# Kernel tuning notes

Hardware: AMD Instinct MI355X
Metric: run time of the kernel (lower is better)

Reference implementation:

```python
import jax, jax.numpy as jnp
import numpy as np

H, W, DIM, B, K = 28, 28, 384, 64, 1
EPS = 1e-5


def setup_inputs() -> dict:
    key = jax.random.key(0)
    k1, k2, k3 = jax.random.split(key, 3)
    L = 1 + K * H * W
    x = jax.random.normal(k1, (B, L, DIM), dtype=jnp.float32)
    w_reduction = jax.random.normal(k2, (2 * DIM, 4 * DIM), dtype=jnp.float32) * 0.02
    w_convert = jax.random.normal(k3, (2 * DIM, DIM), dtype=jnp.float32) * 0.02
    ln_gamma = jnp.ones((4 * DIM,), dtype=jnp.float32)
    ln_beta = jnp.zeros((4 * DIM,), dtype=jnp.float32)
    return {"x": x, "w_reduction": w_reduction, "w_convert": w_convert,
            "ln_gamma": ln_gamma, "ln_beta": ln_beta}


def reference(x, w_reduction, w_convert, ln_gamma, ln_beta):
    Bb, L, C = x.shape
    k = (L - 1) // (H * W)
    cls_token = x[:, 0:1, :]                      # [B,1,C]
    feat = x[:, 1:, :].reshape(Bb, k, H, W, C)
    x0 = feat[:, :, 0::2, 0::2, :]                # [B,k,H/2,W/2,C]
    x1 = feat[:, :, 1::2, 0::2, :]
    x2 = feat[:, :, 0::2, 1::2, :]
    x3 = feat[:, :, 1::2, 1::2, :]
    m = jnp.concatenate([x0, x1, x2, x3], axis=-1)  # [B,k,H/2,W/2,4C]
    m = m.reshape(Bb, k, -1, 4 * C)
    # LayerNorm over last dim
    mu = jnp.mean(m, axis=-1, keepdims=True)
    var = jnp.mean(jnp.square(m - mu), axis=-1, keepdims=True)
    m = (m - mu) * jax.lax.rsqrt(var + EPS) * ln_gamma + ln_beta
    red = jnp.einsum('bknf,of->bkno', m, w_reduction).reshape(Bb, -1, 2 * C)
    cls_out = jnp.einsum('bic,oc->bio', cls_token, w_convert)  # [B,1,2C]
    return jnp.concatenate([cls_out, red], axis=1)
```

## Files before the change

### kernel.cpp

```cpp
#include <hip/hip_runtime.h>
#include <hip/hip_bf16.h>

#define DIMC 384
#define LL 785
#define FDIM 1536
#define ODIM 768
#define NPATCH 196
#define MROWS 12544
#define BATCH 64

typedef __attribute__((ext_vector_type(8))) short bf16x8;
typedef __attribute__((ext_vector_type(4))) float floatx4;
typedef __attribute__((ext_vector_type(4))) unsigned short ushort4v;

#define WS_WBF_OFF  38535168
#define WS_PST_OFF  40894464
#define WS_B2_OFF   41295872

#define PB_CLS   0
#define PB_CAST  192
#define PB_BIAS  3328
#define PB_WBF   3520
#define PREP_BLOCKS 4672

__device__ __forceinline__ unsigned short f2bf(float f) {
  union { float f; unsigned int u; } v; v.f = f;
  unsigned int u = v.u + 0x7fffu + ((v.u >> 16) & 1u);
  return (unsigned short)(u >> 16);
}

__device__ __forceinline__ void gload_lds16(const void* g, void* l) {
  __builtin_amdgcn_global_load_lds(
      (const __attribute__((address_space(1))) unsigned int*)g,
      (__attribute__((address_space(3))) unsigned int*)l, 16, 0, 0);
}

__global__ __launch_bounds__(256) void prep_kernel(
    const float* __restrict__ x, const float* __restrict__ wred,
    const float* __restrict__ wconv, const float* __restrict__ gamma,
    const float* __restrict__ beta, unsigned short* __restrict__ xbf,
    unsigned short* __restrict__ wbf, float2* __restrict__ pst,
    float2* __restrict__ bias2, float* __restrict__ out) {
  const int blk = blockIdx.x;
  const int t = threadIdx.x;
  const int wv = t >> 6;
  const int lane = t & 63;

  if (blk >= PB_CAST && blk < PB_BIAS) {
    const int w = (blk - PB_CAST) * 4 + wv;
    const int vid = w * 4 + (lane >> 4);
    const int sub = lane & 15;
    const int b = vid / 784;
    const int ll = vid - b * 784;
    const float* src = x + ((size_t)b * LL + 1 + ll) * DIMC;
    unsigned short* dst = xbf + (size_t)vid * DIMC;
    float s = 0.f, s2 = 0.f;
#pragma unroll
    for (int c = 0; c < 6; ++c) {
      int f = sub * 4 + c * 64;
      float4 v = *reinterpret_cast<const float4*>(src + f);
      s  += v.x + v.y + v.z + v.w;
      s2 += v.x * v.x + v.y * v.y + v.z * v.z + v.w * v.w;
      union { ushort4v u4; __hip_bfloat162 h[2]; } u;
      u.h[0] = __float22bfloat162_rn(make_float2(v.x, v.y));
      u.h[1] = __float22bfloat162_rn(make_float2(v.z, v.w));
      *reinterpret_cast<ushort4v*>(dst + f) = u.u4;
    }
#pragma unroll
    for (int o = 1; o < 16; o <<= 1) {
      s  += __shfl_xor(s, o);
      s2 += __shfl_xor(s2, o);
    }
    if (sub == 0) pst[vid] = make_float2(s, s2);
  } else if (blk < PB_CAST) {
    __shared__ float xs[DIMC];
    int idx = blk;
    int b = idx / 3;
    int ch = idx - b * 3;
    for (int c = t; c < DIMC; c += 256) xs[c] = x[(size_t)b * LL * DIMC + c];
    __syncthreads();
    int o = ch * 256 + t;
    const float* wr = wconv + (size_t)o * DIMC;
    float a0 = 0.f, a1 = 0.f;
#pragma unroll 4
    for (int c = 0; c < DIMC; c += 8) {
      float4 w0 = *reinterpret_cast<const float4*>(wr + c);
      float4 w1 = *reinterpret_cast<const float4*>(wr + c + 4);
      float4 p0 = *reinterpret_cast<const float4*>(&xs[c]);
      float4 p1 = *reinterpret_cast<const float4*>(&xs[c + 4]);
      a0 += w0.x * p0.x + w0.y * p0.y + w0.z * p0.z + w0.w * p0.w;
      a1 += w1.x * p1.x + w1.y * p1.y + w1.z * p1.z + w1.w * p1.w;
    }
    out[(size_t)b * 197 * ODIM + o] = a0 + a1;
  } else if (blk < PB_WBF) {
    int o = (blk - PB_BIAS) * 4 + wv;
    const float* wr = wred + (size_t)o * FDIM;
    float sb = 0.f, sg = 0.f;
#pragma unroll
    for (int c = 0; c < 6; ++c) {
      int f = lane * 4 + c * 256;
      float4 w = *reinterpret_cast<const float4*>(wr + f);
      float4 be = *reinterpret_cast<const float4*>(beta + f);
      float4 ga = *reinterpret_cast<const float4*>(gamma + f);
      sb += w.x * be.x + w.y * be.y + w.z * be.z + w.w * be.w;
      sg += w.x * ga.x + w.y * ga.y + w.z * ga.z + w.w * ga.w;
    }
#pragma unroll
    for (int o2 = 32; o2 > 0; o2 >>= 1) {
      sb += __shfl_down(sb, o2);
      sg += __shfl_down(sg, o2);
    }
    if (lane == 0) bias2[o] = make_float2(sg, sb);
  } else {
    int idx4 = (blk - PB_WBF) * 256 + t;
    int e0 = idx4 * 4;
    int f = e0 % FDIM;
    float4 w = *reinterpret_cast<const float4*>(wred + e0);
    float4 g = *reinterpret_cast<const float4*>(gamma + f);
    ushort4v u;
    u.x = f2bf(w.x * g.x); u.y = f2bf(w.y * g.y);
    u.z = f2bf(w.z * g.z); u.w = f2bf(w.w * g.w);
    *reinterpret_cast<ushort4v*>(wbf + e0) = u;
  }
}

__global__ __launch_bounds__(256) void gemm_kernel(
    const unsigned short* __restrict__ xbf,
    const unsigned short* __restrict__ wbf,
    const float2* __restrict__ pst, const float2* __restrict__ bias2,
    float* __restrict__ out) {
  __shared__ unsigned short As[128 * 64];
  __shared__ unsigned short Bs[128 * 64];
  __shared__ float2 st[128];

  const int t = threadIdx.x;

  const int NWG = (ODIM / 128) * (MROWS / 128);
  const int qq = NWG >> 3, rr = NWG & 7;
  int bid = blockIdx.x;
  int xcd = bid & 7, pos = bid >> 3;
  int wg = (xcd < rr) ? xcd * (qq + 1) + pos
                      : rr * (qq + 1) + (xcd - rr) * qq + pos;
  int my = wg / 6;
  int nx = wg - my * 6;
  const int mBase = my * 128;
  const int nBase = nx * 128;

  if (t < 128) {
    int m = mBase + t;
    int b = m / NPATCH;
    int n = m - b * NPATCH;
    int i = n / 14;
    int j = n - i * 14;
    int base = b * 784 + i * 56 + j * 2;
    float2 p0 = pst[base];
    float2 p1 = pst[base + 28];
    float2 p2 = pst[base + 1];
    float2 p3 = pst[base + 29];
    float s = p0.x + p1.x + p2.x + p3.x;
    float s2 = p0.y + p1.y + p2.y + p3.y;
    float mu = s * (1.f / FDIM);
    float var = s2 * (1.f / FDIM) - mu * mu;
    float rs = rsqrtf(var + 1e-5f);
    st[t] = make_float2(rs, -mu * rs);
  }

  const unsigned short* agp[4];
  const unsigned short* bgp[4];
  unsigned int ldsoff[4];
#pragma unroll
  for (int p = 0; p < 4; ++p) {
    int s = p * 256 + t;
    int r = s >> 3;
    int cs = (s & 7) ^ (r & 7);
    int m = mBase + r;
    int b = m / NPATCH;
    int n = m - b * NPATCH;
    int i = n / 14;
    int j = n - i * 14;
    agp[p] = xbf + ((size_t)b * 784 + i * 56 + j * 2) * DIMC + cs * 8;
    bgp[p] = wbf + (size_t)(nBase + r) * FDIM + cs * 8;
    ldsoff[p] = (unsigned)s * 8;
  }

  const int wv = t >> 6;
  const int lane = t & 63;
  const int ln15 = lane & 15;
  const int quad = lane >> 4;
  const int wm = wv >> 1;
  const int wn = wv & 1;

  unsigned int aoff[4][2], boff[4][2];
#pragma unroll
  for (int mt = 0; mt < 4; ++mt) {
#pragma unroll
    for (int h = 0; h < 2; ++h) {
      int rA = wm * 64 + mt * 16 + ln15;
      aoff[mt][h] = (unsigned)(rA * 64 + (((h * 4 + quad) ^ (rA & 7)) * 8));
      int rB = wn * 64 + mt * 16 + ln15;
      boff[mt][h] = (unsigned)(rB * 64 + (((h * 4 + quad) ^ (rB & 7)) * 8));
    }
  }

  floatx4 acc[4][4];
#pragma unroll
  for (int mt = 0; mt < 4; ++mt)
#pragma unroll
    for (int nt = 0; nt < 4; ++nt)
      acc[mt][nt] = floatx4{0.f, 0.f, 0.f, 0.f};

  for (int kt = 0; kt < FDIM / 64; ++kt) {
    int q = kt / 6;
    int kk = kt - q * 6;
    int ao = ((q & 1) * 28 + ((q >> 1) & 1)) * DIMC + kk * 64;
    if (kt) __syncthreads();
#pragma unroll
    for (int p = 0; p < 4; ++p) {
      gload_lds16(agp[p] + ao, &As[ldsoff[p]]);
      gload_lds16(bgp[p], &Bs[ldsoff[p]]);
      bgp[p] += 64;
    }
    __syncthreads();

#pragma unroll
    for (int h = 0; h < 2; ++h) {
      bf16x8 af[4], bfr[4];
#pragma unroll
      for (int mt = 0; mt < 4; ++mt)
        af[mt] = *reinterpret_cast<const bf16x8*>(&As[aoff[mt][h]]);
#pragma unroll
      for (int nt = 0; nt < 4; ++nt)
        bfr[nt] = *reinterpret_cast<const bf16x8*>(&Bs[boff[nt][h]]);
#pragma unroll
      for (int mt = 0; mt < 4; ++mt)
#pragma unroll
        for (int nt = 0; nt < 4; ++nt)
          acc[mt][nt] = __builtin_amdgcn_mfma_f32_16x16x32_bf16(
              af[mt], bfr[nt], acc[mt][nt], 0, 0, 0);
    }
  }

  float2 gb[4];
#pragma unroll
  for (int nt = 0; nt < 4; ++nt)
    gb[nt] = bias2[nBase + wn * 64 + nt * 16 + ln15];
#pragma unroll
  for (int mt = 0; mt < 4; ++mt) {
#pragma unroll
    for (int r = 0; r < 4; ++r) {
      int rloc = wm * 64 + mt * 16 + quad * 4 + r;
      float2 sn = st[rloc];
      int m = mBase + rloc;
      int b = m / NPATCH;
      int n = m - b * NPATCH;
      float* orow = out + ((size_t)b * 197 + 1 + n) * ODIM + nBase + wn * 64;
#pragma unroll
      for (int nt = 0; nt < 4; ++nt) {
        float val = fmaf(acc[mt][nt][r], sn.x,
                         fmaf(sn.y, gb[nt].x, gb[nt].y));
        __builtin_nontemporal_store(val, &orow[nt * 16 + ln15]);
      }
    }
  }
}

extern "C" void kernel_launch(void* const* d_in, const int* in_sizes, int n_in,
                              void* d_out, int out_size, void* d_ws, size_t ws_size,
                              hipStream_t stream) {
  const float* x     = (const float*)d_in[0];
  const float* wred  = (const float*)d_in[1];
  const float* wconv = (const float*)d_in[2];
  const float* gamma = (const float*)d_in[3];
  const float* beta  = (const float*)d_in[4];
  float* out = (float*)d_out;

  unsigned short* xbf = (unsigned short*)d_ws;
  unsigned short* wbf = (unsigned short*)((char*)d_ws + WS_WBF_OFF);
  float2* pst         = (float2*)((char*)d_ws + WS_PST_OFF);
  float2* bias2       = (float2*)((char*)d_ws + WS_B2_OFF);

  prep_kernel<<<dim3(PREP_BLOCKS), 256, 0, stream>>>(x, wred, wconv, gamma,
                                                     beta, xbf, wbf, pst,
                                                     bias2, out);
  gemm_kernel<<<dim3((ODIM / 128) * (MROWS / 128)), 256, 0, stream>>>(
      xbf, wbf, pst, bias2, out);
}
```

Before: 174.1 us.

## Shrink GEMM N-tile to 64 for more workgroups; cast two rows per lane-group

The GEMM output tile goes from 128x128 to 128x64, doubling the workgroup count from 588 to 1176 so the 256 CUs are better filled, with a simplified XCD-aware mapping. Per-wave accumulators drop from 16 to 8 MFMA tiles, and the B LDS buffer is halved. Separately, the prep cast kernel now handles two rows per 16-lane group: it issues all loads before the bf16 stores and writes the paired stats as one float4, halving the block count. The smaller tile means more A-tile reloads, so the A matrix is fetched twice as often overall, and there is less MFMA work per LDS load.

```diff
diff --git a/kernel.cpp b/kernel.cpp
--- a/kernel.cpp
+++ b/kernel.cpp
@@ -19,9 +19,9 @@
 
 #define PB_CLS   0
 #define PB_CAST  192
-#define PB_BIAS  3328
-#define PB_WBF   3520
-#define PREP_BLOCKS 4672
+#define PB_BIAS  1760
+#define PB_WBF   1952
+#define PREP_BLOCKS 3104
 
 __device__ __forceinline__ unsigned short f2bf(float f) {
   union { float f; unsigned int u; } v; v.f = f;
@@ -48,30 +48,49 @@
 
   if (blk >= PB_CAST && blk < PB_BIAS) {
     const int w = (blk - PB_CAST) * 4 + wv;
-    const int vid = w * 4 + (lane >> 4);
+    const int vid0 = w * 8 + (lane >> 4) * 2;
     const int sub = lane & 15;
-    const int b = vid / 784;
-    const int ll = vid - b * 784;
-    const float* src = x + ((size_t)b * LL + 1 + ll) * DIMC;
-    unsigned short* dst = xbf + (size_t)vid * DIMC;
-    float s = 0.f, s2 = 0.f;
-#pragma unroll
-    for (int c = 0; c < 6; ++c) {
-      int f = sub * 4 + c * 64;
-      float4 v = *reinterpret_cast<const float4*>(src + f);
-      s  += v.x + v.y + v.z + v.w;
-      s2 += v.x * v.x + v.y * v.y + v.z * v.z + v.w * v.w;
-      union { ushort4v u4; __hip_bfloat162 h[2]; } u;
-      u.h[0] = __float22bfloat162_rn(make_float2(v.x, v.y));
-      u.h[1] = __float22bfloat162_rn(make_float2(v.z, v.w));
-      *reinterpret_cast<ushort4v*>(dst + f) = u.u4;
+    float4 v[2][6];
+    float s[2], s2[2];
+#pragma unroll
+    for (int r = 0; r < 2; ++r) {
+      int vid = vid0 + r;
+      int b = vid / 784;
+      int ll = vid - b * 784;
+      const float* src = x + ((size_t)b * LL + 1 + ll) * DIMC;
+      s[r] = 0.f; s2[r] = 0.f;
+#pragma unroll
+      for (int c = 0; c < 6; ++c) {
+        float4 vv = *reinterpret_cast<const float4*>(src + sub * 4 + c * 64);
+        v[r][c] = vv;
+        s[r]  += vv.x + vv.y + vv.z + vv.w;
+        s2[r] += vv.x * vv.x + vv.y * vv.y + vv.z * vv.z + vv.w * vv.w;
+      }
+    }
+#pragma unroll
+    for (int r = 0; r < 2; ++r) {
+      unsigned short* dst = xbf + (size_t)(vid0 + r) * DIMC;
+#pragma unroll
+      for (int c = 0; c < 6; ++c) {
+        float4 vv = v[r][c];
+        union { ushort4v u4; __hip_bfloat162 h[2]; } u;
+        u.h[0] = __float22bfloat162_rn(make_float2(vv.x, vv.y));
+        u.h[1] = __float22bfloat162_rn(make_float2(vv.z, vv.w));
+        *reinterpret_cast<ushort4v*>(dst + sub * 4 + c * 64) = u.u4;
+      }
     }
 #pragma unroll
     for (int o = 1; o < 16; o <<= 1) {
-      s  += __shfl_xor(s, o);
-      s2 += __shfl_xor(s2, o);
-    }
-    if (sub == 0) pst[vid] = make_float2(s, s2);
+#pragma unroll
+      for (int r = 0; r < 2; ++r) {
+        s[r]  += __shfl_xor(s[r], o);
+        s2[r] += __shfl_xor(s2[r], o);
+      }
+    }
+    if (sub == 0) {
+      float4 pp = make_float4(s[0], s2[0], s[1], s2[1]);
+      *reinterpret_cast<float4*>(&pst[vid0]) = pp;
+    }
   } else if (blk < PB_CAST) {
     __shared__ float xs[DIMC];
     int idx = blk;
@@ -130,21 +149,17 @@
     const float2* __restrict__ pst, const float2* __restrict__ bias2,
     float* __restrict__ out) {
   __shared__ unsigned short As[128 * 64];
-  __shared__ unsigned short Bs[128 * 64];
+  __shared__ unsigned short Bs[64 * 64];
   __shared__ float2 st[128];
 
   const int t = threadIdx.x;
 
-  const int NWG = (ODIM / 128) * (MROWS / 128);
-  const int qq = NWG >> 3, rr = NWG & 7;
   int bid = blockIdx.x;
-  int xcd = bid & 7, pos = bid >> 3;
-  int wg = (xcd < rr) ? xcd * (qq + 1) + pos
-                      : rr * (qq + 1) + (xcd - rr) * qq + pos;
-  int my = wg / 6;
-  int nx = wg - my * 6;
+  int wg = (bid & 7) * 147 + (bid >> 3);
+  int my = wg / 12;
+  int nx = wg - my * 12;
   const int mBase = my * 128;
-  const int nBase = nx * 128;
+  const int nBase = nx * 64;
 
   if (t < 128) {
     int m = mBase + t;
@@ -166,8 +181,8 @@
   }
 
   const unsigned short* agp[4];
-  const unsigned short* bgp[4];
-  unsigned int ldsoff[4];
+  const unsigned short* bgp[2];
+  unsigned int aldso[4], bldso[2];
 #pragma unroll
   for (int p = 0; p < 4; ++p) {
     int s = p * 256 + t;
@@ -179,8 +194,15 @@
     int i = n / 14;
     int j = n - i * 14;
     agp[p] = xbf + ((size_t)b * 784 + i * 56 + j * 2) * DIMC + cs * 8;
+    aldso[p] = (unsigned)s * 8;
+  }
+#pragma unroll
+  for (int p = 0; p < 2; ++p) {
+    int s = p * 256 + t;
+    int r = s >> 3;
+    int cs = (s & 7) ^ (r & 7);
     bgp[p] = wbf + (size_t)(nBase + r) * FDIM + cs * 8;
-    ldsoff[p] = (unsigned)s * 8;
+    bldso[p] = (unsigned)s * 8;
   }
 
   const int wv = t >> 6;
@@ -190,23 +212,27 @@
   const int wm = wv >> 1;
   const int wn = wv & 1;
 
-  unsigned int aoff[4][2], boff[4][2];
-#pragma unroll
-  for (int mt = 0; mt < 4; ++mt) {
+  unsigned int aoff[4][2], boff[2][2];
+#pragma unroll
+  for (int mt = 0; mt < 4; ++mt)
 #pragma unroll
     for (int h = 0; h < 2; ++h) {
       int rA = wm * 64 + mt * 16 + ln15;
       aoff[mt][h] = (unsigned)(rA * 64 + (((h * 4 + quad) ^ (rA & 7)) * 8));
-      int rB = wn * 64 + mt * 16 + ln15;
-      boff[mt][h] = (unsigned)(rB * 64 + (((h * 4 + quad) ^ (rB & 7)) * 8));
-    }
-  }
-
-  floatx4 acc[4][4];
+    }
+#pragma unroll
+  for (int nt = 0; nt < 2; ++nt)
+#pragma unroll
+    for (int h = 0; h < 2; ++h) {
+      int rB = wn * 32 + nt * 16 + ln15;
+      boff[nt][h] = (unsigned)(rB * 64 + (((h * 4 + quad) ^ (rB & 7)) * 8));
+    }
+
+  floatx4 acc[4][2];
 #pragma unroll
   for (int mt = 0; mt < 4; ++mt)
 #pragma unroll
-    for (int nt = 0; nt < 4; ++nt)
+    for (int nt = 0; nt < 2; ++nt)
       acc[mt][nt] = floatx4{0.f, 0.f, 0.f, 0.f};
 
   for (int kt = 0; kt < FDIM / 64; ++kt) {
@@ -215,35 +241,37 @@
     int ao = ((q & 1) * 28 + ((q >> 1) & 1)) * DIMC + kk * 64;
     if (kt) __syncthreads();
 #pragma unroll
-    for (int p = 0; p < 4; ++p) {
-      gload_lds16(agp[p] + ao, &As[ldsoff[p]]);
-      gload_lds16(bgp[p], &Bs[ldsoff[p]]);
+    for (int p = 0; p < 4; ++p)
+      gload_lds16(agp[p] + ao, &As[aldso[p]]);
+#pragma unroll
+    for (int p = 0; p < 2; ++p) {
+      gload_lds16(bgp[p], &Bs[bldso[p]]);
       bgp[p] += 64;
     }
     __syncthreads();
 
 #pragma unroll
     for (int h = 0; h < 2; ++h) {
-      bf16x8 af[4], bfr[4];
+      bf16x8 af[4], bfr[2];
 #pragma unroll
       for (int mt = 0; mt < 4; ++mt)
         af[mt] = *reinterpret_cast<const bf16x8*>(&As[aoff[mt][h]]);
 #pragma unroll
-      for (int nt = 0; nt < 4; ++nt)
+      for (int nt = 0; nt < 2; ++nt)
         bfr[nt] = *reinterpret_cast<const bf16x8*>(&Bs[boff[nt][h]]);
 #pragma unroll
       for (int mt = 0; mt < 4; ++mt)
 #pragma unroll
-        for (int nt = 0; nt < 4; ++nt)
+        for (int nt = 0; nt < 2; ++nt)
           acc[mt][nt] = __builtin_amdgcn_mfma_f32_16x16x32_bf16(
               af[mt], bfr[nt], acc[mt][nt], 0, 0, 0);
     }
   }
 
-  float2 gb[4];
-#pragma unroll
-  for (int nt = 0; nt < 4; ++nt)
-    gb[nt] = bias2[nBase + wn * 64 + nt * 16 + ln15];
+  float2 gb[2];
+#pragma unroll
+  for (int nt = 0; nt < 2; ++nt)
+    gb[nt] = bias2[nBase + wn * 32 + nt * 16 + ln15];
 #pragma unroll
   for (int mt = 0; mt < 4; ++mt) {
 #pragma unroll
@@ -253,9 +281,9 @@
       int m = mBase + rloc;
       int b = m / NPATCH;
       int n = m - b * NPATCH;
-      float* orow = out + ((size_t)b * 197 + 1 + n) * ODIM + nBase + wn * 64;
-#pragma unroll
-      for (int nt = 0; nt < 4; ++nt) {
+      float* orow = out + ((size_t)b * 197 + 1 + n) * ODIM + nBase + wn * 32;
+#pragma unroll
+      for (int nt = 0; nt < 2; ++nt) {
         float val = fmaf(acc[mt][nt][r], sn.x,
                          fmaf(sn.y, gb[nt].x, gb[nt].y));
         __builtin_nontemporal_store(val, &orow[nt * 16 + ln15]);
@@ -282,6 +310,5 @@
   prep_kernel<<<dim3(PREP_BLOCKS), 256, 0, stream>>>(x, wred, wconv, gamma,
                                                      beta, xbf, wbf, pst,
                                                      bias2, out);
-  gemm_kernel<<<dim3((ODIM / 128) * (MROWS / 128)), 256, 0, stream>>>(
-      xbf, wbf, pst, bias2, out);
-}
+  gemm_kernel<<<dim3(1176), 256, 0, stream>>>(xbf, wbf, pst, bias2, out);
+}
```

After: 178.1 us. +2.3%, slower.

## Fuse fp32-to-bf16 activation cast and LayerNorm stats into GEMM A-loading

Applied to the files above, without the earlier changes.

Removes the separate prep pass that cast x to bf16 and computed per-token sums. The GEMM now reads fp32 x directly through registers, converts it to bf16, stores it to LDS, and accumulates row sum and sum-of-squares for the LayerNorm statistics. The next tile's A loads are issued early so they overlap the MFMA work. This avoids writing and re-reading a bf16 copy of x, but fp32 A reads are twice as wide and each x row is read by six column-tile blocks. It also costs extra registers and drops the direct global-to-LDS path for A.

```diff
diff --git a/kernel.cpp b/kernel.cpp
--- a/kernel.cpp
+++ b/kernel.cpp
@@ -13,15 +13,12 @@
 typedef __attribute__((ext_vector_type(4))) float floatx4;
 typedef __attribute__((ext_vector_type(4))) unsigned short ushort4v;
 
-#define WS_WBF_OFF  38535168
-#define WS_PST_OFF  40894464
-#define WS_B2_OFF   41295872
+#define WS_B2_OFF 2359296
 
 #define PB_CLS   0
-#define PB_CAST  192
-#define PB_BIAS  3328
-#define PB_WBF   3520
-#define PREP_BLOCKS 4672
+#define PB_BIAS  192
+#define PB_WBF   384
+#define PREP_BLOCKS 1536
 
 __device__ __forceinline__ unsigned short f2bf(float f) {
   union { float f; unsigned int u; } v; v.f = f;
@@ -38,41 +35,14 @@
 __global__ __launch_bounds__(256) void prep_kernel(
     const float* __restrict__ x, const float* __restrict__ wred,
     const float* __restrict__ wconv, const float* __restrict__ gamma,
-    const float* __restrict__ beta, unsigned short* __restrict__ xbf,
-    unsigned short* __restrict__ wbf, float2* __restrict__ pst,
+    const float* __restrict__ beta, unsigned short* __restrict__ wbf,
     float2* __restrict__ bias2, float* __restrict__ out) {
   const int blk = blockIdx.x;
   const int t = threadIdx.x;
   const int wv = t >> 6;
   const int lane = t & 63;
 
-  if (blk >= PB_CAST && blk < PB_BIAS) {
-    const int w = (blk - PB_CAST) * 4 + wv;
-    const int vid = w * 4 + (lane >> 4);
-    const int sub = lane & 15;
-    const int b = vid / 784;
-    const int ll = vid - b * 784;
-    const float* src = x + ((size_t)b * LL + 1 + ll) * DIMC;
-    unsigned short* dst = xbf + (size_t)vid * DIMC;
-    float s = 0.f, s2 = 0.f;
-#pragma unroll
-    for (int c = 0; c < 6; ++c) {
-      int f = sub * 4 + c * 64;
-      float4 v = *reinterpret_cast<const float4*>(src + f);
-      s  += v.x + v.y + v.z + v.w;
-      s2 += v.x * v.x + v.y * v.y + v.z * v.z + v.w * v.w;
-      union { ushort4v u4; __hip_bfloat162 h[2]; } u;
-      u.h[0] = __float22bfloat162_rn(make_float2(v.x, v.y));
-      u.h[1] = __float22bfloat162_rn(make_float2(v.z, v.w));
-      *reinterpret_cast<ushort4v*>(dst + f) = u.u4;
-    }
-#pragma unroll
-    for (int o = 1; o < 16; o <<= 1) {
-      s  += __shfl_xor(s, o);
-      s2 += __shfl_xor(s2, o);
-    }
-    if (sub == 0) pst[vid] = make_float2(s, s2);
-  } else if (blk < PB_CAST) {
+  if (blk < PB_BIAS) {
     __shared__ float xs[DIMC];
     int idx = blk;
     int b = idx / 3;
@@ -125,10 +95,9 @@
 }
 
 __global__ __launch_bounds__(256) void gemm_kernel(
-    const unsigned short* __restrict__ xbf,
+    const float* __restrict__ x,
     const unsigned short* __restrict__ wbf,
-    const float2* __restrict__ pst, const float2* __restrict__ bias2,
-    float* __restrict__ out) {
+    const float2* __restrict__ bias2, float* __restrict__ out) {
   __shared__ unsigned short As[128 * 64];
   __shared__ unsigned short Bs[128 * 64];
   __shared__ float2 st[128];
@@ -146,28 +115,9 @@
   const int mBase = my * 128;
   const int nBase = nx * 128;
 
-  if (t < 128) {
-    int m = mBase + t;
-    int b = m / NPATCH;
-    int n = m - b * NPATCH;
-    int i = n / 14;
-    int j = n - i * 14;
-    int base = b * 784 + i * 56 + j * 2;
-    float2 p0 = pst[base];
-    float2 p1 = pst[base + 28];
-    float2 p2 = pst[base + 1];
-    float2 p3 = pst[base + 29];
-    float s = p0.x + p1.x + p2.x + p3.x;
-    float s2 = p0.y + p1.y + p2.y + p3.y;
-    float mu = s * (1.f / FDIM);
-    float var = s2 * (1.f / FDIM) - mu * mu;
-    float rs = rsqrtf(var + 1e-5f);
-    st[t] = make_float2(rs, -mu * rs);
-  }
-
-  const unsigned short* agp[4];
+  const float* agp[4];
   const unsigned short* bgp[4];
-  unsigned int ldsoff[4];
+  unsigned int ldso[4];
 #pragma unroll
   for (int p = 0; p < 4; ++p) {
     int s = p * 256 + t;
@@ -178,9 +128,9 @@
     int n = m - b * NPATCH;
     int i = n / 14;
     int j = n - i * 14;
-    agp[p] = xbf + ((size_t)b * 784 + i * 56 + j * 2) * DIMC + cs * 8;
+    agp[p] = x + ((size_t)b * LL + 1 + i * 56 + j * 2) * DIMC + cs * 8;
     bgp[p] = wbf + (size_t)(nBase + r) * FDIM + cs * 8;
-    ldsoff[p] = (unsigned)s * 8;
+    ldso[p] = (unsigned)s * 8;
   }
 
   const int wv = t >> 6;
@@ -209,18 +159,50 @@
     for (int nt = 0; nt < 4; ++nt)
       acc[mt][nt] = floatx4{0.f, 0.f, 0.f, 0.f};
 
+  float4 av0[4], av1[4];
+  float sr[4], s2r[4];
+#pragma unroll
+  for (int p = 0; p < 4; ++p) { sr[p] = 0.f; s2r[p] = 0.f; }
+
+#pragma unroll
+  for (int p = 0; p < 4; ++p) {
+    av0[p] = *reinterpret_cast<const float4*>(agp[p]);
+    av1[p] = *reinterpret_cast<const float4*>(agp[p] + 4);
+  }
+
   for (int kt = 0; kt < FDIM / 64; ++kt) {
-    int q = kt / 6;
-    int kk = kt - q * 6;
-    int ao = ((q & 1) * 28 + ((q >> 1) & 1)) * DIMC + kk * 64;
     if (kt) __syncthreads();
 #pragma unroll
     for (int p = 0; p < 4; ++p) {
-      gload_lds16(agp[p] + ao, &As[ldsoff[p]]);
-      gload_lds16(bgp[p], &Bs[ldsoff[p]]);
+      float4 v0 = av0[p], v1 = av1[p];
+      sr[p]  += v0.x + v0.y + v0.z + v0.w + v1.x + v1.y + v1.z + v1.w;
+      s2r[p] += v0.x * v0.x + v0.y * v0.y + v0.z * v0.z + v0.w * v0.w
+              + v1.x * v1.x + v1.y * v1.y + v1.z * v1.z + v1.w * v1.w;
+      union { bf16x8 b8; __hip_bfloat162 h[4]; } u;
+      u.h[0] = __float22bfloat162_rn(make_float2(v0.x, v0.y));
+      u.h[1] = __float22bfloat162_rn(make_float2(v0.z, v0.w));
+      u.h[2] = __float22bfloat162_rn(make_float2(v1.x, v1.y));
+      u.h[3] = __float22bfloat162_rn(make_float2(v1.z, v1.w));
+      *reinterpret_cast<bf16x8*>(&As[ldso[p]]) = u.b8;
+    }
+#pragma unroll
+    for (int p = 0; p < 4; ++p) {
+      gload_lds16(bgp[p], &Bs[ldso[p]]);
       bgp[p] += 64;
     }
     __syncthreads();
+
+    if (kt + 1 < FDIM / 64) {
+      int ktn = kt + 1;
+      int q = ktn / 6;
+      int kk = ktn - q * 6;
+      int ao = ((q & 1) * 28 + ((q >> 1) & 1)) * DIMC + kk * 64;
+#pragma unroll
+      for (int p = 0; p < 4; ++p) {
+        av0[p] = *reinterpret_cast<const float4*>(agp[p] + ao);
+        av1[p] = *reinterpret_cast<const float4*>(agp[p] + ao + 4);
+      }
+    }
 
 #pragma unroll
     for (int h = 0; h < 2; ++h) {
@@ -239,6 +221,25 @@
               af[mt], bfr[nt], acc[mt][nt], 0, 0, 0);
     }
   }
+
+#pragma unroll
+  for (int p = 0; p < 4; ++p) {
+#pragma unroll
+    for (int o = 1; o < 8; o <<= 1) {
+      sr[p]  += __shfl_xor(sr[p], o);
+      s2r[p] += __shfl_xor(s2r[p], o);
+    }
+  }
+  if ((t & 7) == 0) {
+#pragma unroll
+    for (int p = 0; p < 4; ++p) {
+      float mu = sr[p] * (1.f / FDIM);
+      float var = s2r[p] * (1.f / FDIM) - mu * mu;
+      float rs = rsqrtf(var + 1e-5f);
+      st[p * 32 + (t >> 3)] = make_float2(rs, -mu * rs);
+    }
+  }
+  __syncthreads();
 
   float2 gb[4];
 #pragma unroll
@@ -274,14 +275,11 @@
   const float* beta  = (const float*)d_in[4];
   float* out = (float*)d_out;
 
-  unsigned short* xbf = (unsigned short*)d_ws;
-  unsigned short* wbf = (unsigned short*)((char*)d_ws + WS_WBF_OFF);
-  float2* pst         = (float2*)((char*)d_ws + WS_PST_OFF);
+  unsigned short* wbf = (unsigned short*)d_ws;
   float2* bias2       = (float2*)((char*)d_ws + WS_B2_OFF);
 
   prep_kernel<<<dim3(PREP_BLOCKS), 256, 0, stream>>>(x, wred, wconv, gamma,
-                                                     beta, xbf, wbf, pst,
-                                                     bias2, out);
+                                                     beta, wbf, bias2, out);
   gemm_kernel<<<dim3((ODIM / 128) * (MROWS / 128)), 256, 0, stream>>>(
-      xbf, wbf, pst, bias2, out);
-}
+      x, wbf, bias2, out);
+}
```

Result: slower. 208.6 us (+19.8%).
